# Performance work log

Hardware: AMD Instinct MI355X
Metric: run time of the kernel (lower is better)

The kernel has to match this reference:

```python
import jax, jax.numpy as jnp
import numpy as np

N, E, B = 60000, 360000, 64        # nodes, edges, graphs
IN_DIM, HID, L, NCLS = 256, 512, 3, 1000
EPS = 1e-5                          # BatchNorm1d eps


def setup_inputs() -> dict:
    key = jax.random.key(0)
    ks = jax.random.split(key, 10)
    s = 0.05
    x = jax.random.normal(ks[0], (N, IN_DIM), dtype=jnp.float32)
    edge_index = jax.random.randint(ks[1], (2, E), 0, N, dtype=jnp.int32)
    batch = jnp.sort(jax.random.randint(ks[2], (N,), 0, B, dtype=jnp.int32))
    W_embed = jax.random.normal(ks[3], (IN_DIM, HID), dtype=jnp.float32) * s
    # per-block params (all 3 blocks have identical shapes -> stacked on axis 0)
    W1 = jax.random.normal(ks[4], (L, 2 * HID, HID), dtype=jnp.float32) * s
    b1 = jnp.zeros((L, HID), jnp.float32)
    g1 = jnp.ones((L, HID), jnp.float32)
    be1 = jnp.zeros((L, HID), jnp.float32)
    W2 = jax.random.normal(ks[5], (L, 2 * HID, HID), dtype=jnp.float32) * s
    b2 = jnp.zeros((L, HID), jnp.float32)
    g2 = jnp.ones((L, HID), jnp.float32)
    be2 = jnp.zeros((L, HID), jnp.float32)
    W_att = jax.random.normal(ks[6], (HID, 1), dtype=jnp.float32) * s
    W_read = jax.random.normal(ks[7], (HID, NCLS), dtype=jnp.float32) * s
    return dict(x=x, edge_index=edge_index, batch=batch, W_embed=W_embed,
                W1=W1, b1=b1, g1=g1, be1=be1, W2=W2, b2=b2, g2=g2, be2=be2,
                W_att=W_att, W_read=W_read)


def _segment_mean(vals, idx, num):
    s = jax.ops.segment_sum(vals, idx, num_segments=num)
    c = jax.ops.segment_sum(jnp.ones((vals.shape[0], 1), vals.dtype), idx, num_segments=num)
    return s / jnp.maximum(c, 1.0)


def _bn(h, g, b):  # BatchNorm1d, training-mode batch statistics (biased var)
    m = h.mean(0)
    v = jnp.mean((h - m) ** 2, axis=0)
    return (h - m) * jax.lax.rsqrt(v + EPS) * g + b


def _sage(h, src, dst, W, b):
    # MySAGEConv (position=False -> message = x_j), aggr='mean', concat=True, L2 normalize
    aggr = _segment_mean(h[src], dst, h.shape[0])          # [N, d] mean of neighbor msgs
    out = jnp.concatenate([h, aggr], axis=-1) @ W + b      # [N, 2d] @ [2d, d]
    norm = jnp.linalg.norm(out, axis=-1, keepdims=True)
    return out / jnp.maximum(norm, 1e-12)                  # F.normalize(p=2)


def reference(x, edge_index, batch, W_embed, W1, b1, g1, be1,
              W2, b2, g2, be2, W_att, W_read):
    src, dst = edge_index[0], edge_index[1]
    h = x @ W_embed
    for l in range(L):  # MySAGEConvBlock, gcn_num=2, has_linear_in_block=False
        identity = h
        out = jax.nn.relu(_bn(_sage(h, src, dst, W1[l], b1[l]), g1[l], be1[l]))
        out = jax.nn.relu(_bn(_sage(out, src, dst, W2[l], b2[l]), g2[l], be2[l]))
        h = out + identity  # residual (dims match)
    # AttentionClass
    att = jax.nn.sigmoid(h @ W_att)           # [N, 1]
    hx = (att * h + h) * 0.5
    hg = _segment_mean(hx, batch, B)          # global mean pool per graph
    return hg @ W_read                        # [B, 1000] logits
```

## Files before the change

### kernel.cpp

```cpp
#include <hip/hip_runtime.h>
#include <math.h>

#define N_NODES 60000
#define N_EDGES 360000
#define N_GRAPH 64
#define HID 512
#define NCLS 1000
#define BN_EPS 1e-5f
#define NS ((size_t)N_NODES * HID)
#define NB 235
#define STRIPS 469

typedef __bf16 bf16x8 __attribute__((ext_vector_type(8)));
typedef float f32x4 __attribute__((ext_vector_type(4)));

static __device__ __forceinline__ unsigned short f2bf(float f) {
  unsigned u = __float_as_uint(f);
  unsigned r = (u + 0x7fffu + ((u >> 16) & 1u)) >> 16;
  return (unsigned short)r;
}
static __device__ __forceinline__ float bfLo(unsigned u) { return __uint_as_float(u << 16); }
static __device__ __forceinline__ float bfHi(unsigned u) { return __uint_as_float(u & 0xffff0000u); }
static __device__ __forceinline__ unsigned packbf(float a, float b) {
  return (unsigned)f2bf(a) | ((unsigned)f2bf(b) << 16);
}

__global__ void write_sentinel(float* out, float v) { out[0] = v; }

__global__ __launch_bounds__(256) void cvt_bf16(const float* __restrict__ X,
                                                unsigned short* __restrict__ Y,
                                                long n4) {
  long i = (long)blockIdx.x * 256 + threadIdx.x;
  if (i >= n4) return;
  float4 f = *(const float4*)(X + i * 4);
  uint2 o;
  o.x = packbf(f.x, f.y);
  o.y = packbf(f.z, f.w);
  *(uint2*)(Y + i * 4) = o;
}

__global__ __launch_bounds__(256) void wtrans(const float* __restrict__ W,
                                              unsigned short* __restrict__ Wt,
                                              int K, int N) {
  __shared__ float sh[32][33];
  int kt = blockIdx.x * 32, nt = blockIdx.y * 32;
  int tx = threadIdx.x & 31, ty = threadIdx.x >> 5;
#pragma unroll
  for (int i = 0; i < 4; ++i)
    sh[ty + i * 8][tx] = W[(size_t)(kt + ty + i * 8) * N + nt + tx];
  __syncthreads();
#pragma unroll
  for (int i = 0; i < 4; ++i)
    Wt[(size_t)(nt + ty + i * 8) * K + kt + tx] = f2bf(sh[tx][ty + i * 8]);
}

__global__ __launch_bounds__(256) void count_deg(const int* __restrict__ dst,
                                                 int* __restrict__ deg, int E) {
  int e = blockIdx.x * 256 + threadIdx.x;
  if (e < E) atomicAdd(&deg[dst[e]], 1);
}

__global__ __launch_bounds__(256) void make_invdeg(const int* __restrict__ deg,
                                                   float* __restrict__ inv, int n) {
  int i = blockIdx.x * 256 + threadIdx.x;
  if (i < n) inv[i] = 1.0f / fmaxf((float)deg[i], 1.0f);
}

__global__ __launch_bounds__(256) void scan_part(const int* __restrict__ deg,
                                                 int* __restrict__ bsum, int n) {
  __shared__ int sh[256];
  int i = blockIdx.x * 256 + threadIdx.x;
  sh[threadIdx.x] = (i < n) ? deg[i] : 0;
  __syncthreads();
  for (int off = 128; off; off >>= 1) {
    if (threadIdx.x < off) sh[threadIdx.x] += sh[threadIdx.x + off];
    __syncthreads();
  }
  if (threadIdx.x == 0) bsum[blockIdx.x] = sh[0];
}

__global__ __launch_bounds__(256) void scan_bsums(int* __restrict__ bsum, int nb) {
  __shared__ int sh[256];
  int t = threadIdx.x;
  int v = (t < nb) ? bsum[t] : 0;
  sh[t] = v;
  __syncthreads();
  for (int off = 1; off < 256; off <<= 1) {
    int u = (t >= off) ? sh[t - off] : 0;
    __syncthreads();
    sh[t] += u;
    __syncthreads();
  }
  if (t < nb) bsum[t] = sh[t] - v;
}

__global__ __launch_bounds__(256) void scan_final(const int* __restrict__ deg,
                                                  const int* __restrict__ bsum,
                                                  int* __restrict__ rowptr, int n) {
  __shared__ int sh[256];
  int t = threadIdx.x;
  int i = blockIdx.x * 256 + t;
  int v = (i < n) ? deg[i] : 0;
  sh[t] = v;
  __syncthreads();
  for (int off = 1; off < 256; off <<= 1) {
    int u = (t >= off) ? sh[t - off] : 0;
    __syncthreads();
    sh[t] += u;
    __syncthreads();
  }
  if (i < n) rowptr[i + 1] = bsum[blockIdx.x] + sh[t];
  if (i == 0) rowptr[0] = 0;
}

__global__ __launch_bounds__(256) void fill_csr(const int* __restrict__ src,
                                                const int* __restrict__ dst,
                                                const int* __restrict__ rowptr,
                                                int* __restrict__ fillc,
                                                int* __restrict__ esrc, int E) {
  int e = blockIdx.x * 256 + threadIdx.x;
  if (e < E) {
    int d = dst[e];
    int pos = rowptr[d] + atomicAdd(&fillc[d], 1);
    esrc[pos] = src[e];
  }
}

__global__ __launch_bounds__(256) void bcount(const int* __restrict__ batch,
                                              float* __restrict__ bcnt, int n) {
  __shared__ int h[N_GRAPH];
  if (threadIdx.x < N_GRAPH) h[threadIdx.x] = 0;
  __syncthreads();
  int i = blockIdx.x * 256 + threadIdx.x;
  if (i < n) atomicAdd(&h[batch[i]], 1);
  __syncthreads();
  if (threadIdx.x < N_GRAPH && h[threadIdx.x])
    atomicAdd(&bcnt[threadIdx.x], (float)h[threadIdx.x]);
}

#define GEMM_BODY(Xb, ldx, Wtb, ldw, bias_p, outp, KDIM)                        \
  const int wv = tid >> 6, lane = tid & 63;                                     \
  const int wm = (wv >> 1) * 64, wn = (wv & 1) * 64;                            \
  const int lm = lane & 15, quad = lane >> 4;                                   \
  const int grow = lane & 15, gseg = (lane >> 4) * 8;                           \
  f32x4 zero; zero[0] = 0.f; zero[1] = 0.f; zero[2] = 0.f; zero[3] = 0.f;       \
  f32x4 acc[4][4];                                                              \
  _Pragma("unroll") for (int i = 0; i < 4; ++i)                                 \
    _Pragma("unroll") for (int j = 0; j < 4; ++j) acc[i][j] = zero;             \
  for (int kt = 0; kt < (KDIM); kt += 32) {                                     \
    __syncthreads();                                                            \
    _Pragma("unroll") for (int r = 0; r < 2; ++r) {                             \
      int chunk = wv + r * 4;                                                   \
      int row = chunk * 16 + grow;                                              \
      const unsigned short* ga = (Xb) + (size_t)(bm + row) * (ldx) + kt + gseg; \
      const unsigned short* gb = (Wtb) + (size_t)(bn + row) * (ldw) + kt + gseg;\
      __builtin_amdgcn_global_load_lds(                                         \
          (const __attribute__((address_space(1))) unsigned int*)ga,            \
          (__attribute__((address_space(3))) unsigned int*)(As + chunk * 512),  \
          16, 0, 0);                                                            \
      __builtin_amdgcn_global_load_lds(                                         \
          (const __attribute__((address_space(1))) unsigned int*)gb,            \
          (__attribute__((address_space(3))) unsigned int*)(Bs + chunk * 512),  \
          16, 0, 0);                                                            \
    }                                                                           \
    __syncthreads();                                                            \
    bf16x8 af[4], bfr[4];                                                       \
    _Pragma("unroll") for (int i = 0; i < 4; ++i)                               \
      af[i] = *(const bf16x8*)(As + (wm / 16 + i) * 512 + lane * 8);            \
    _Pragma("unroll") for (int j = 0; j < 4; ++j)                               \
      bfr[j] = *(const bf16x8*)(Bs + (wn / 16 + j) * 512 + lane * 8);           \
    _Pragma("unroll") for (int i = 0; i < 4; ++i)                               \
      _Pragma("unroll") for (int j = 0; j < 4; ++j)                             \
        acc[i][j] = __builtin_amdgcn_mfma_f32_16x16x32_bf16(af[i], bfr[j],      \
                                                            acc[i][j], 0, 0, 0);\
  }                                                                             \
  const int qr = quad * 4;                                                      \
  const int rl = tid >> 4, seg = (tid & 15) * 8;                                \
  _Pragma("unroll") for (int p = 0; p < 2; ++p) {                               \
    __syncthreads();                                                            \
    if ((wv >> 1) == p) {                                                       \
      _Pragma("unroll") for (int j = 0; j < 4; ++j) {                           \
        int col = wn + j * 16 + lm;                                             \
        float bvv = (bias_p) ? (bias_p)[bn + col] : 0.f;                        \
        _Pragma("unroll") for (int i = 0; i < 4; ++i)                           \
          _Pragma("unroll") for (int r = 0; r < 4; ++r)                         \
            Cs[i * 16 + qr + r][col] = f2bf(acc[i][j][r] + bvv);                \
      }                                                                         \
    }                                                                           \
    __syncthreads();                                                            \
    _Pragma("unroll") for (int pass = 0; pass < 4; ++pass) {                    \
      int row = bm + p * 64 + pass * 16 + rl;                                   \
      if (row < M)                                                              \
        *(uint4*)((outp) + (size_t)row * 512 + bn + seg) =                      \
            *(const uint4*)(&Cs[pass * 16 + rl][seg]);                          \
    }                                                                           \
  }

__global__ __launch_bounds__(256) void gemm_glds(
    const unsigned short* __restrict__ Xb, int ldx, int K,
    const unsigned short* __restrict__ Wt, int ldw,
    const float* __restrict__ bias,
    unsigned short* __restrict__ outB, int M) {
  __shared__ __align__(16) unsigned short As[128 * 32];
  __shared__ __align__(16) unsigned short Bs[128 * 32];
  __shared__ __align__(16) unsigned short Cs[64][136];
  const int tid = threadIdx.x;
  const int L = blockIdx.x;
  const int xcd = L & 7, li = L >> 3;
  const int strip = xcd * 59 + (li >> 2);
  if (strip >= STRIPS) return;
  const int bm = strip * 128;
  const int bn = (li & 3) * 128;
  GEMM_BODY(Xb, ldx, Wt, ldw, bias, outB, K)
}

__global__ __launch_bounds__(256) void gemm_dual(
    const unsigned short* __restrict__ Xb, int ldx,
    const unsigned short* __restrict__ Wt,
    const float* __restrict__ biasA,
    unsigned short* __restrict__ outA, unsigned short* __restrict__ outBf,
    int M) {
  __shared__ __align__(16) unsigned short As[128 * 32];
  __shared__ __align__(16) unsigned short Bs[128 * 32];
  __shared__ __align__(16) unsigned short Cs[64][136];
  const int tid = threadIdx.x;
  const int L = blockIdx.x;
  const int xcd = L & 7, li = L >> 3;
  const int strip = xcd * 59 + (li >> 3);
  if (strip >= STRIPS) return;
  const int cb = li & 7;
  const int bm = strip * 128;
  const int bn = (cb & 3) * 128;
  const unsigned short* Wtb = Wt + (cb < 4 ? 0 : 512);
  const float* bias = (cb < 4) ? biasA : nullptr;
  unsigned short* outp = (cb < 4) ? outA : outBf;
  GEMM_BODY(Xb, ldx, Wtb, 1024, bias, outp, 512)
}

__global__ __launch_bounds__(512) void gemm_strip(
    const unsigned short* __restrict__ Xb, int ldx,
    const unsigned short* __restrict__ Wt, int ldw,
    const float* __restrict__ bias,
    unsigned short* __restrict__ outB, int M) {
  __shared__ __align__(16) unsigned short As[64][40];
  const int tid = threadIdx.x;
  const int bm = blockIdx.x * 64;
  const int wv = tid >> 6, lane = tid & 63;
  const int lm = lane & 15, quad = lane >> 4, lk = quad * 8;
  const int cb = wv * 64;
  const int arow = tid >> 3, aseg = (tid & 7) * 4;

  f32x4 zero;
  zero[0] = 0.f; zero[1] = 0.f; zero[2] = 0.f; zero[3] = 0.f;
  f32x4 acc[4][4];
#pragma unroll
  for (int i = 0; i < 4; ++i)
#pragma unroll
    for (int j = 0; j < 4; ++j) acc[i][j] = zero;

  for (int kt = 0; kt < 512; kt += 32) {
    uint2 av = make_uint2(0, 0);
    int gr = bm + arow;
    if (gr < M) av = *(const uint2*)(Xb + (size_t)gr * ldx + kt + aseg);
    bf16x8 bfr[4];
#pragma unroll
    for (int j = 0; j < 4; ++j)
      bfr[j] = *(const bf16x8*)(Wt + (size_t)(cb + j * 16 + lm) * ldw + kt + lk);
    __syncthreads();
    *(uint2*)(&As[arow][aseg]) = av;
    __syncthreads();
    bf16x8 af[4];
#pragma unroll
    for (int i = 0; i < 4; ++i) af[i] = *(const bf16x8*)(&As[i * 16 + lm][lk]);
#pragma unroll
    for (int i = 0; i < 4; ++i)
#pragma unroll
      for (int j = 0; j < 4; ++j)
        acc[i][j] = __builtin_amdgcn_mfma_f32_16x16x32_bf16(af[i], bfr[j], acc[i][j], 0, 0, 0);
  }

  const int qr = quad * 4;
#pragma unroll
  for (int j = 0; j < 4; ++j) {
    int col = cb + j * 16 + lm;
    float bvv = bias ? bias[col] : 0.f;
#pragma unroll
    for (int i = 0; i < 4; ++i) {
      int rbase = bm + i * 16 + qr;
#pragma unroll
      for (int r = 0; r < 4; ++r) {
        int row = rbase + r;
        if (row < M) outB[(size_t)row * 512 + col] = f2bf(acc[i][j][r] + bvv);
      }
    }
  }
}

__global__ __launch_bounds__(256) void aggr_norm_stats(
    unsigned short* __restrict__ Ya, const unsigned short* __restrict__ Yb,
    const int* __restrict__ rowptr, const int* __restrict__ esrc,
    const float* __restrict__ invdeg, float* __restrict__ sums, int M) {
  __shared__ float ps[4][1024];
  const int tid = threadIdx.x;
  const int w = tid >> 6, lane = tid & 63;
  float s[8] = {}, q[8] = {};
  const int base = blockIdx.x * 64 + w * 16;
  for (int n = 0; n < 16; ++n) {
    int d = base + n;
    if (d >= M) break;
    float acc[8] = {0.f, 0.f, 0.f, 0.f, 0.f, 0.f, 0.f, 0.f};
    int beg = rowptr[d], end = rowptr[d + 1];
    for (int e = beg; e < end; ++e) {
      int src = esrc[e];
      uint4 u = *(const uint4*)(Yb + (size_t)src * 512 + lane * 8);
      acc[0] += bfLo(u.x); acc[1] += bfHi(u.x);
      acc[2] += bfLo(u.y); acc[3] += bfHi(u.y);
      acc[4] += bfLo(u.z); acc[5] += bfHi(u.z);
      acc[6] += bfLo(u.w); acc[7] += bfHi(u.w);
    }
    float iv = invdeg[d];
    uint4 a = *(const uint4*)(Ya + (size_t)d * 512 + lane * 8);
    float r0 = bfLo(a.x) + iv * acc[0], r1 = bfHi(a.x) + iv * acc[1];
    float r2 = bfLo(a.y) + iv * acc[2], r3 = bfHi(a.y) + iv * acc[3];
    float r4 = bfLo(a.z) + iv * acc[4], r5 = bfHi(a.z) + iv * acc[5];
    float r6 = bfLo(a.w) + iv * acc[6], r7 = bfHi(a.w) + iv * acc[7];
    float ss = r0 * r0 + r1 * r1 + r2 * r2 + r3 * r3
             + r4 * r4 + r5 * r5 + r6 * r6 + r7 * r7;
#pragma unroll
    for (int o = 32; o; o >>= 1) ss += __shfl_xor(ss, o, 64);
    float inv = 1.0f / fmaxf(sqrtf(ss), 1e-12f);
    float v[8] = {r0 * inv, r1 * inv, r2 * inv, r3 * inv,
                  r4 * inv, r5 * inv, r6 * inv, r7 * inv};
#pragma unroll
    for (int k = 0; k < 8; ++k) { s[k] += v[k]; q[k] += v[k] * v[k]; }
    uint4 o4;
    o4.x = packbf(v[0], v[1]); o4.y = packbf(v[2], v[3]);
    o4.z = packbf(v[4], v[5]); o4.w = packbf(v[6], v[7]);
    *(uint4*)(Ya + (size_t)d * 512 + lane * 8) = o4;
  }
#pragma unroll
  for (int k = 0; k < 8; ++k) {
    ps[w][lane * 8 + k] = s[k];
    ps[w][512 + lane * 8 + k] = q[k];
  }
  __syncthreads();
  int c4 = tid * 4;
#pragma unroll
  for (int j = 0; j < 4; ++j) {
    float tot = ps[0][c4 + j] + ps[1][c4 + j] + ps[2][c4 + j] + ps[3][c4 + j];
    atomicAdd(&sums[c4 + j], tot);
  }
}

__global__ __launch_bounds__(256) void bn_apply(const unsigned short* __restrict__ U,
                                                unsigned short* __restrict__ H,
                                                const float* __restrict__ sums,
                                                const float* __restrict__ g,
                                                const float* __restrict__ be,
                                                int M, int residual) {
  size_t i2 = (size_t)blockIdx.x * 256 + threadIdx.x;
  if (i2 >= NS / 2) return;
  int c = ((int)(i2 & 255)) * 2;
  float invM = 1.0f / (float)M;
  float m0 = sums[c] * invM, m1 = sums[c + 1] * invM;
  float v0 = sums[512 + c] * invM - m0 * m0;
  float v1 = sums[512 + c + 1] * invM - m1 * m1;
  float k0 = rsqrtf(v0 + BN_EPS) * g[c], k1 = rsqrtf(v1 + BN_EPS) * g[c + 1];
  unsigned u = ((const unsigned*)U)[i2];
  float x0 = fmaxf((bfLo(u) - m0) * k0 + be[c], 0.f);
  float x1 = fmaxf((bfHi(u) - m1) * k1 + be[c + 1], 0.f);
  if (residual) {
    unsigned hv = ((const unsigned*)H)[i2];
    x0 += bfLo(hv);
    x1 += bfHi(hv);
  }
  ((unsigned*)H)[i2] = packbf(x0, x1);
}

#define NPB 64
__global__ __launch_bounds__(256) void att_pool2(const unsigned short* __restrict__ H,
                                                 const int* __restrict__ batch,
                                                 const float* __restrict__ Watt,
                                                 float* __restrict__ hg, int M) {
  __shared__ float fsh[NPB];
  __shared__ int bsh[NPB];
  const int tid = threadIdx.x;
  const int base = blockIdx.x * NPB;
  if (tid < NPB) bsh[tid] = (base + tid < M) ? batch[base + tid] : -1;
  const int wv = tid >> 6, lane = tid & 63;
  float4 wa0 = *(const float4*)(Watt + lane * 8);
  float4 wa1 = *(const float4*)(Watt + lane * 8 + 4);
  __syncthreads();
  for (int i = wv; i < NPB; i += 4) {
    int node = base + i;
    float dot = 0.f;
    if (node < M) {
      uint4 u = *(const uint4*)(H + (size_t)node * 512 + lane * 8);
      dot = bfLo(u.x) * wa0.x + bfHi(u.x) * wa0.y
          + bfLo(u.y) * wa0.z + bfHi(u.y) * wa0.w
          + bfLo(u.z) * wa1.x + bfHi(u.z) * wa1.y
          + bfLo(u.w) * wa1.z + bfHi(u.w) * wa1.w;
    }
#pragma unroll
    for (int o = 32; o; o >>= 1) dot += __shfl_xor(dot, o, 64);
    if (lane == 0) fsh[i] = 0.5f * (1.0f + 1.0f / (1.0f + expf(-dot)));
  }
  __syncthreads();
  float a0 = 0.f, a1 = 0.f;
  int cur = bsh[0];
  for (int i = 0; i < NPB; ++i) {
    int node = base + i;
    if (node >= M) break;
    int b = bsh[i];
    if (b != cur) {
      atomicAdd(&hg[(size_t)cur * 512 + tid * 2], a0);
      atomicAdd(&hg[(size_t)cur * 512 + tid * 2 + 1], a1);
      a0 = a1 = 0.f;
      cur = b;
    }
    unsigned u = *(const unsigned*)(H + (size_t)node * 512 + tid * 2);
    float f = fsh[i];
    a0 += bfLo(u) * f;
    a1 += bfHi(u) * f;
  }
  if (cur >= 0) {
    atomicAdd(&hg[(size_t)cur * 512 + tid * 2], a0);
    atomicAdd(&hg[(size_t)cur * 512 + tid * 2 + 1], a1);
  }
}

__global__ __launch_bounds__(256) void readout(const float* __restrict__ hg,
                                               const float* __restrict__ bcnt,
                                               const float* __restrict__ Wr,
                                               float* __restrict__ out) {
  __shared__ float sh[HID];
  int g = blockIdx.x;
  int n = blockIdx.y * 256 + threadIdx.x;
  float inv = 1.0f / fmaxf(bcnt[g], 1.0f);
  for (int k = threadIdx.x; k < HID; k += 256) sh[k] = hg[(size_t)g * HID + k] * inv;
  __syncthreads();
  if (n < NCLS) {
    float acc = 0.f;
    for (int k = 0; k < HID; ++k) acc += sh[k] * Wr[(size_t)k * NCLS + n];
    out[(size_t)g * NCLS + n] = acc;
  }
}

extern "C" void kernel_launch(void* const* d_in, const int* in_sizes, int n_in,
                              void* d_out, int out_size, void* d_ws, size_t ws_size,
                              hipStream_t stream) {
  const float* x       = (const float*)d_in[0];
  const int*   ei      = (const int*)d_in[1];
  const int*   batch   = (const int*)d_in[2];
  const float* W_embed = (const float*)d_in[3];
  const float* W1      = (const float*)d_in[4];
  const float* b1      = (const float*)d_in[5];
  const float* g1      = (const float*)d_in[6];
  const float* be1     = (const float*)d_in[7];
  const float* W2      = (const float*)d_in[8];
  const float* b2      = (const float*)d_in[9];
  const float* g2      = (const float*)d_in[10];
  const float* be2     = (const float*)d_in[11];
  const float* Watt    = (const float*)d_in[12];
  const float* Wread   = (const float*)d_in[13];
  float* out = (float*)d_out;

  const int* srcIdx = ei;
  const int* dstIdx = ei + N_EDGES;

  char* p = (char*)d_ws;
  unsigned short* B0 = (unsigned short*)p; p += NS * 2;
  unsigned short* B1 = (unsigned short*)p; p += NS * 2;
  unsigned short* B2 = (unsigned short*)p; p += NS * 2;
  unsigned short* WtE = (unsigned short*)p; p += (size_t)512 * 256 * 2;
  unsigned short* Wt1 = (unsigned short*)p; p += (size_t)3 * 512 * 1024 * 2;
  unsigned short* Wt2 = (unsigned short*)p; p += (size_t)3 * 512 * 1024 * 2;
  float* hg     = (float*)p; p += (size_t)N_GRAPH * HID * 4;
  float* sums   = (float*)p; p += 1024 * 4;
  float* invdeg = (float*)p; p += (size_t)N_NODES * 4;
  float* bcnt   = (float*)p; p += 256;
  int* deg      = (int*)p;   p += (size_t)N_NODES * 4;
  int* fillc    = (int*)p;   p += (size_t)N_NODES * 4;
  int* esrc     = (int*)p;   p += (size_t)N_EDGES * 4;
  int* rowptr   = (int*)p;   p += (size_t)(N_NODES + 1) * 4;
  int* bsum     = (int*)p;   p += (size_t)NB * 4;
  size_t need = (size_t)(p - (char*)d_ws);
  if (ws_size < need) {
    write_sentinel<<<1, 1, 0, stream>>>(out, (float)need);
    return;
  }

  wtrans<<<dim3(8, 16), 256, 0, stream>>>(W_embed, WtE, 256, 512);
  for (int l = 0; l < 3; ++l) {
    wtrans<<<dim3(32, 16), 256, 0, stream>>>(W1 + (size_t)l * 1024 * 512,
                                             Wt1 + (size_t)l * 512 * 1024, 1024, 512);
    wtrans<<<dim3(32, 16), 256, 0, stream>>>(W2 + (size_t)l * 1024 * 512,
                                             Wt2 + (size_t)l * 512 * 1024, 1024, 512);
  }

  hipMemsetAsync(deg, 0, N_NODES * sizeof(int), stream);
  hipMemsetAsync(fillc, 0, N_NODES * sizeof(int), stream);
  count_deg<<<(N_EDGES + 255) / 256, 256, 0, stream>>>(dstIdx, deg, N_EDGES);
  make_invdeg<<<(N_NODES + 255) / 256, 256, 0, stream>>>(deg, invdeg, N_NODES);
  scan_part<<<NB, 256, 0, stream>>>(deg, bsum, N_NODES);
  scan_bsums<<<1, 256, 0, stream>>>(bsum, NB);
  scan_final<<<NB, 256, 0, stream>>>(deg, bsum, rowptr, N_NODES);
  fill_csr<<<(N_EDGES + 255) / 256, 256, 0, stream>>>(srcIdx, dstIdx, rowptr, fillc,
                                                      esrc, N_EDGES);

  const int g1grid = 8 * 59 * 4;
  const int g2grid = 8 * 59 * 8;
  const int sgrid  = (N_NODES + 63) / 64;
  const int agrid  = (N_NODES + 63) / 64;
  const int egrid  = (int)((NS / 2 + 255) / 256);

  cvt_bf16<<<(int)(((size_t)N_NODES * 64 + 255) / 256), 256, 0, stream>>>(
      x, B1, (long)N_NODES * 64);
  gemm_glds<<<g1grid, 256, 0, stream>>>(B1, 256, 256, WtE, 256, nullptr, B0, N_NODES);

  for (int l = 0; l < 3; ++l) {
    const unsigned short* Wt1l = Wt1 + (size_t)l * 512 * 1024;
    const unsigned short* Wt2l = Wt2 + (size_t)l * 512 * 1024;
    hipMemsetAsync(sums, 0, 1024 * sizeof(float), stream);
    gemm_dual<<<g2grid, 256, 0, stream>>>(B0, 512, Wt1l, b1 + l * 512, B1, B2, N_NODES);
    aggr_norm_stats<<<agrid, 256, 0, stream>>>(B1, B2, rowptr, esrc, invdeg,
                                               sums, N_NODES);
    bn_apply<<<egrid, 256, 0, stream>>>(B1, B1, sums, g1 + l * 512,
                                        be1 + l * 512, N_NODES, 0);
    hipMemsetAsync(sums, 0, 1024 * sizeof(float), stream);
    gemm_glds<<<g1grid, 256, 0, stream>>>(B1, 512, 512, Wt2l + 512, 1024,
                                          nullptr, B2, N_NODES);
    gemm_strip<<<sgrid, 512, 0, stream>>>(B1, 512, Wt2l, 1024,
                                          b2 + l * 512, B1, N_NODES);
    aggr_norm_stats<<<agrid, 256, 0, stream>>>(B1, B2, rowptr, esrc, invdeg,
                                               sums, N_NODES);
    bn_apply<<<egrid, 256, 0, stream>>>(B1, B0, sums, g2 + l * 512,
                                        be2 + l * 512, N_NODES, 1);
  }

  hipMemsetAsync(hg, 0, (size_t)N_GRAPH * HID * sizeof(float), stream);
  hipMemsetAsync(bcnt, 0, N_GRAPH * sizeof(float), stream);
  bcount<<<NB, 256, 0, stream>>>(batch, bcnt, N_NODES);
  att_pool2<<<(N_NODES + NPB - 1) / NPB, 256, 0, stream>>>(B0, batch, Watt, hg, N_NODES);
  readout<<<dim3(N_GRAPH, 4), 256, 0, stream>>>(hg, bcnt, Wread, out);
}
```

Measured before the change: 2.421 ms.

## Split aggregation from BN statistics into separate gather and column-reduction kernels

The fused gather+normalize+stats kernel, where each wave handled 16 nodes, becomes a one-node-per-wave aggregation kernel with many more blocks. Column sums and sums of squares move to a separate bn_stats pass that re-reads the normalized bf16 output, and the sums buffer is now cleared just before that pass. The aim is more parallelism and latency hiding in the irregular gather, at the cost of an extra full read of the N×512 activation and an extra launch per layer half. The statistics are now taken from the bf16-rounded values rather than the fp32 ones.

```diff
diff --git a/kernel.cpp b/kernel.cpp
--- a/kernel.cpp
+++ b/kernel.cpp
@@ -296,60 +296,57 @@
   }
 }
 
-__global__ __launch_bounds__(256) void aggr_norm_stats(
+__global__ __launch_bounds__(256) void aggr_norm(
     unsigned short* __restrict__ Ya, const unsigned short* __restrict__ Yb,
     const int* __restrict__ rowptr, const int* __restrict__ esrc,
-    const float* __restrict__ invdeg, float* __restrict__ sums, int M) {
-  __shared__ float ps[4][1024];
-  const int tid = threadIdx.x;
-  const int w = tid >> 6, lane = tid & 63;
-  float s[8] = {}, q[8] = {};
-  const int base = blockIdx.x * 64 + w * 16;
-  for (int n = 0; n < 16; ++n) {
-    int d = base + n;
-    if (d >= M) break;
-    float acc[8] = {0.f, 0.f, 0.f, 0.f, 0.f, 0.f, 0.f, 0.f};
-    int beg = rowptr[d], end = rowptr[d + 1];
-    for (int e = beg; e < end; ++e) {
-      int src = esrc[e];
-      uint4 u = *(const uint4*)(Yb + (size_t)src * 512 + lane * 8);
-      acc[0] += bfLo(u.x); acc[1] += bfHi(u.x);
-      acc[2] += bfLo(u.y); acc[3] += bfHi(u.y);
-      acc[4] += bfLo(u.z); acc[5] += bfHi(u.z);
-      acc[6] += bfLo(u.w); acc[7] += bfHi(u.w);
-    }
-    float iv = invdeg[d];
-    uint4 a = *(const uint4*)(Ya + (size_t)d * 512 + lane * 8);
-    float r0 = bfLo(a.x) + iv * acc[0], r1 = bfHi(a.x) + iv * acc[1];
-    float r2 = bfLo(a.y) + iv * acc[2], r3 = bfHi(a.y) + iv * acc[3];
-    float r4 = bfLo(a.z) + iv * acc[4], r5 = bfHi(a.z) + iv * acc[5];
-    float r6 = bfLo(a.w) + iv * acc[6], r7 = bfHi(a.w) + iv * acc[7];
-    float ss = r0 * r0 + r1 * r1 + r2 * r2 + r3 * r3
-             + r4 * r4 + r5 * r5 + r6 * r6 + r7 * r7;
-#pragma unroll
-    for (int o = 32; o; o >>= 1) ss += __shfl_xor(ss, o, 64);
-    float inv = 1.0f / fmaxf(sqrtf(ss), 1e-12f);
-    float v[8] = {r0 * inv, r1 * inv, r2 * inv, r3 * inv,
-                  r4 * inv, r5 * inv, r6 * inv, r7 * inv};
-#pragma unroll
-    for (int k = 0; k < 8; ++k) { s[k] += v[k]; q[k] += v[k] * v[k]; }
-    uint4 o4;
-    o4.x = packbf(v[0], v[1]); o4.y = packbf(v[2], v[3]);
-    o4.z = packbf(v[4], v[5]); o4.w = packbf(v[6], v[7]);
-    *(uint4*)(Ya + (size_t)d * 512 + lane * 8) = o4;
-  }
-#pragma unroll
-  for (int k = 0; k < 8; ++k) {
-    ps[w][lane * 8 + k] = s[k];
-    ps[w][512 + lane * 8 + k] = q[k];
-  }
-  __syncthreads();
-  int c4 = tid * 4;
-#pragma unroll
-  for (int j = 0; j < 4; ++j) {
-    float tot = ps[0][c4 + j] + ps[1][c4 + j] + ps[2][c4 + j] + ps[3][c4 + j];
-    atomicAdd(&sums[c4 + j], tot);
-  }
+    const float* __restrict__ invdeg, int M) {
+  int d = blockIdx.x * 4 + (threadIdx.x >> 6);
+  int lane = threadIdx.x & 63;
+  if (d >= M) return;
+  float acc[8] = {0.f, 0.f, 0.f, 0.f, 0.f, 0.f, 0.f, 0.f};
+  int beg = rowptr[d], end = rowptr[d + 1];
+  for (int e = beg; e < end; ++e) {
+    int s = esrc[e];
+    uint4 u = *(const uint4*)(Yb + (size_t)s * 512 + lane * 8);
+    acc[0] += bfLo(u.x); acc[1] += bfHi(u.x);
+    acc[2] += bfLo(u.y); acc[3] += bfHi(u.y);
+    acc[4] += bfLo(u.z); acc[5] += bfHi(u.z);
+    acc[6] += bfLo(u.w); acc[7] += bfHi(u.w);
+  }
+  float iv = invdeg[d];
+  uint4 a = *(const uint4*)(Ya + (size_t)d * 512 + lane * 8);
+  float r0 = bfLo(a.x) + iv * acc[0], r1 = bfHi(a.x) + iv * acc[1];
+  float r2 = bfLo(a.y) + iv * acc[2], r3 = bfHi(a.y) + iv * acc[3];
+  float r4 = bfLo(a.z) + iv * acc[4], r5 = bfHi(a.z) + iv * acc[5];
+  float r6 = bfLo(a.w) + iv * acc[6], r7 = bfHi(a.w) + iv * acc[7];
+  float ss = r0 * r0 + r1 * r1 + r2 * r2 + r3 * r3
+           + r4 * r4 + r5 * r5 + r6 * r6 + r7 * r7;
+#pragma unroll
+  for (int o = 32; o; o >>= 1) ss += __shfl_xor(ss, o, 64);
+  float inv = 1.0f / fmaxf(sqrtf(ss), 1e-12f);
+  uint4 o4;
+  o4.x = packbf(r0 * inv, r1 * inv);
+  o4.y = packbf(r2 * inv, r3 * inv);
+  o4.z = packbf(r4 * inv, r5 * inv);
+  o4.w = packbf(r6 * inv, r7 * inv);
+  *(uint4*)(Ya + (size_t)d * 512 + lane * 8) = o4;
+}
+
+__global__ __launch_bounds__(256) void bn_stats(const unsigned short* __restrict__ T,
+                                                int M, float* __restrict__ sums) {
+  const int t = threadIdx.x;
+  int r0 = blockIdx.x * 128;
+  int rend = min(r0 + 128, M);
+  float s0 = 0.f, q0 = 0.f, s1 = 0.f, q1 = 0.f;
+  for (int r = r0; r < rend; ++r) {
+    float a = __uint_as_float((unsigned)T[(size_t)r * 512 + t] << 16);
+    float b = __uint_as_float((unsigned)T[(size_t)r * 512 + t + 256] << 16);
+    s0 += a; q0 += a * a; s1 += b; q1 += b * b;
+  }
+  atomicAdd(&sums[t], s0);
+  atomicAdd(&sums[t + 256], s1);
+  atomicAdd(&sums[512 + t], q0);
+  atomicAdd(&sums[512 + t + 256], q1);
 }
 
 __global__ __launch_bounds__(256) void bn_apply(const unsigned short* __restrict__ U,
@@ -511,7 +508,8 @@
   const int g1grid = 8 * 59 * 4;
   const int g2grid = 8 * 59 * 8;
   const int sgrid  = (N_NODES + 63) / 64;
-  const int agrid  = (N_NODES + 63) / 64;
+  const int ngrid  = (N_NODES + 3) / 4;
+  const int bgrid  = (N_NODES + 127) / 128;
   const int egrid  = (int)((NS / 2 + 255) / 256);
 
   cvt_bf16<<<(int)(((size_t)N_NODES * 64 + 255) / 256), 256, 0, stream>>>(
@@ -521,19 +519,19 @@
   for (int l = 0; l < 3; ++l) {
     const unsigned short* Wt1l = Wt1 + (size_t)l * 512 * 1024;
     const unsigned short* Wt2l = Wt2 + (size_t)l * 512 * 1024;
+    gemm_dual<<<g2grid, 256, 0, stream>>>(B0, 512, Wt1l, b1 + l * 512, B1, B2, N_NODES);
+    aggr_norm<<<ngrid, 256, 0, stream>>>(B1, B2, rowptr, esrc, invdeg, N_NODES);
     hipMemsetAsync(sums, 0, 1024 * sizeof(float), stream);
-    gemm_dual<<<g2grid, 256, 0, stream>>>(B0, 512, Wt1l, b1 + l * 512, B1, B2, N_NODES);
-    aggr_norm_stats<<<agrid, 256, 0, stream>>>(B1, B2, rowptr, esrc, invdeg,
-                                               sums, N_NODES);
+    bn_stats<<<bgrid, 256, 0, stream>>>(B1, N_NODES, sums);
     bn_apply<<<egrid, 256, 0, stream>>>(B1, B1, sums, g1 + l * 512,
                                         be1 + l * 512, N_NODES, 0);
-    hipMemsetAsync(sums, 0, 1024 * sizeof(float), stream);
     gemm_glds<<<g1grid, 256, 0, stream>>>(B1, 512, 512, Wt2l + 512, 1024,
                                           nullptr, B2, N_NODES);
     gemm_strip<<<sgrid, 512, 0, stream>>>(B1, 512, Wt2l, 1024,
                                           b2 + l * 512, B1, N_NODES);
-    aggr_norm_stats<<<agrid, 256, 0, stream>>>(B1, B2, rowptr, esrc, invdeg,
-                                               sums, N_NODES);
+    aggr_norm<<<ngrid, 256, 0, stream>>>(B1, B2, rowptr, esrc, invdeg, N_NODES);
+    hipMemsetAsync(sums, 0, 1024 * sizeof(float), stream);
+    bn_stats<<<bgrid, 256, 0, stream>>>(B1, N_NODES, sums);
     bn_apply<<<egrid, 256, 0, stream>>>(B1, B0, sums, g2 + l * 512,
                                         be2 + l * 512, N_NODES, 1);
   }
```

New measurement: 2.084 ms. -13.9%, faster.
